# Kernel tuning notes

Measured on AMD Instinct MI355X. Metric: run time of the kernel, lower is better.

The kernel has to match this reference:

```python
import jax, jax.numpy as jnp
import numpy as np
from jax import lax


def _conv(x, w, b):
    # x: [B,C,H,W] NCHW, w: [O,I,3,3] OIHW, SAME padding, stride 1
    y = lax.conv_general_dilated(x, w, (1, 1), 'SAME',
                                 dimension_numbers=('NCHW', 'OIHW', 'NCHW'))
    return y + b[None, :, None, None]


def _maxpool2(x):
    return lax.reduce_window(x, -jnp.inf, lax.max,
                             (1, 1, 2, 2), (1, 1, 2, 2), 'VALID')


def _squash(x):
    # x: [..., D]
    norm = jnp.sum(x * x, axis=-1, keepdims=True)
    scale = norm / (1.0 + norm) / jnp.sqrt(norm + 1e-9)
    return scale * x


def _routing(x, W):
    # x: [B, R, C]  (R routes, C in_channels); W: [N, R, C, O]
    # u_hat[b,n,r,o] = sum_c x[b,r,c] * W[n,r,c,o]
    u_hat = jnp.einsum('brc,nrco->bnro', x, W)
    B, N, R, O = u_hat.shape
    b_ij = jnp.zeros((B, N, R), dtype=u_hat.dtype)
    v = None
    for it in range(3):  # fixed 3 routing iterations
        c_ij = jax.nn.softmax(b_ij, axis=2)
        s_j = jnp.einsum('bnr,bnro->bno', c_ij, u_hat)
        v = _squash(s_j)
        if it < 2:
            b_ij = b_ij + jnp.einsum('bnro,bno->bnr', u_hat, v)
    return v  # [B, N, O]


def setup_inputs() -> dict:
    key = jax.random.key(0)
    ks = jax.random.split(key, 10)
    B = 512
    num_classes = 15
    x = jax.random.normal(ks[0], (B, 3, 64, 64), dtype=jnp.float32)

    def kaiming(k, shape, fan_in):
        return jax.random.normal(k, shape, dtype=jnp.float32) * np.sqrt(2.0 / fan_in)

    w1 = kaiming(ks[1], (8, 3, 3, 3), 3 * 9)
    b1 = jnp.zeros((8,), jnp.float32)
    w2 = kaiming(ks[2], (16, 8, 3, 3), 8 * 9)
    b2 = jnp.zeros((16,), jnp.float32)
    w3 = kaiming(ks[3], (32, 16, 3, 3), 16 * 9)
    b3 = jnp.zeros((32,), jnp.float32)
    # route_weights are torch.randn in the original (std 1.0)
    rw1 = jax.random.normal(ks[4], (32, 64, 32, 8), dtype=jnp.float32)   # primary
    rw2 = jax.random.normal(ks[5], (num_classes, 32, 8, 16), dtype=jnp.float32)  # secondary
    fc_w = kaiming(ks[6], (num_classes, 16 * num_classes), 16 * num_classes)
    fc_b = jnp.zeros((num_classes,), jnp.float32)
    return {'x': x, 'w1': w1, 'b1': b1, 'w2': w2, 'b2': b2,
            'w3': w3, 'b3': b3, 'rw1': rw1, 'rw2': rw2,
            'fc_w': fc_w, 'fc_b': fc_b}


def reference(x, w1, b1, w2, b2, w3, b3, rw1, rw2, fc_w, fc_b):
    h = _maxpool2(jax.nn.relu(_conv(x, w1, b1)))   # [B,8,32,32]
    h = _maxpool2(jax.nn.relu(_conv(h, w2, b2)))   # [B,16,16,16]
    h = _maxpool2(jax.nn.relu(_conv(h, w3, b3)))   # [B,32,8,8]
    B = h.shape[0]
    # routes = 64 spatial positions, channels = 32 capsule input features
    feats = h.reshape(B, 32, 64).transpose(0, 2, 1)  # [B, 64, 32]
    v1 = _routing(feats, rw1)   # [B, 32, 8]
    v2 = _routing(v1, rw2)      # [B, 15, 16]
    flat = v2.reshape(B, -1)    # [B, 240]
    return flat @ fc_w.T + fc_b  # [B, 15]
```

## Files before the change

kernel.cpp:

```cpp
#include <hip/hip_runtime.h>
#include <hip/hip_bf16.h>


template<int CIN, int COUT, int HIN, int NO>
__global__ __launch_bounds__(256)
void conv_relu_pool(const float* __restrict__ in, const float* __restrict__ w,
                    const float* __restrict__ bias, float* __restrict__ out)
{
    constexpr int HOUT = HIN / 2;
    constexpr int PR = HIN + 2;
    constexpr int PC = (HIN + 2 + 3) & ~3;
    constexpr int NS = HIN / 8;
    constexpr int NOP = COUT / NO;
    constexpr int NTASK = NOP * HOUT * NS;
    constexpr int XWORDS = CIN * PR * PC;
    constexpr int WWORDS = CIN * 9 * COUT;

    __shared__ float xin[CIN][PR][PC];
    __shared__ float wt[WWORDS];
    __shared__ float bl[COUT];

    const int tid = threadIdx.x;
    const int b   = blockIdx.x;

    for (int i = tid; i < XWORDS; i += 256) ((float*)xin)[i] = 0.f;
    for (int i = tid; i < WWORDS; i += 256) {
        int o = i % COUT, k = (i / COUT) % 9, c = i / (COUT * 9);
        wt[i] = w[(o * CIN + c) * 9 + k];
    }
    if (tid < COUT) bl[tid] = bias[tid];
    __syncthreads();

    const float4* gin = (const float4*)(in + (size_t)b * CIN * HIN * HIN);
    constexpr int CHUNKS = CIN * HIN * (HIN / 4);
    for (int i = tid; i < CHUNKS; i += 256) {
        float4 v = gin[i];
        int ch = i % (HIN / 4);
        int y  = (i / (HIN / 4)) % HIN;
        int c  = i / ((HIN / 4) * HIN);
        float* dst = &xin[c][y + 1][ch * 4 + 1];
        dst[0] = v.x; dst[1] = v.y; dst[2] = v.z; dst[3] = v.w;
    }
    __syncthreads();

    for (int task = tid; task < NTASK; task += 256) {
        const int s  = task % NS;
        const int py = (task / NS) % HOUT;
        const int o0 = (task / (NS * HOUT)) * NO;
        const int X0 = s * 8;

        float acc[NO][2][8];
#pragma unroll
        for (int n = 0; n < NO; ++n)
#pragma unroll
            for (int q = 0; q < 2; ++q)
#pragma unroll
                for (int j = 0; j < 8; ++j) acc[n][q][j] = 0.f;

        for (int c = 0; c < CIN; ++c) {
            float rows[4][12];
#pragma unroll
            for (int rr = 0; rr < 4; ++rr) {
                const float4* src = (const float4*)&xin[c][2 * py + rr][X0];
#pragma unroll
                for (int j = 0; j < 3; ++j) {
                    float4 v = src[j];
                    rows[rr][j * 4 + 0] = v.x; rows[rr][j * 4 + 1] = v.y;
                    rows[rr][j * 4 + 2] = v.z; rows[rr][j * 4 + 3] = v.w;
                }
            }
            const float* wc = wt + c * 9 * COUT;
#pragma unroll
            for (int ky = 0; ky < 3; ++ky) {
#pragma unroll
                for (int n = 0; n < NO; ++n) {
                    const float w0 = wc[(ky * 3 + 0) * COUT + o0 + n];
                    const float w1 = wc[(ky * 3 + 1) * COUT + o0 + n];
                    const float w2 = wc[(ky * 3 + 2) * COUT + o0 + n];
#pragma unroll
                    for (int j = 0; j < 8; ++j) {
                        acc[n][0][j] = fmaf(rows[ky][j],     w0, acc[n][0][j]);
                        acc[n][0][j] = fmaf(rows[ky][j + 1], w1, acc[n][0][j]);
                        acc[n][0][j] = fmaf(rows[ky][j + 2], w2, acc[n][0][j]);
                        acc[n][1][j] = fmaf(rows[ky + 1][j],     w0, acc[n][1][j]);
                        acc[n][1][j] = fmaf(rows[ky + 1][j + 1], w1, acc[n][1][j]);
                        acc[n][1][j] = fmaf(rows[ky + 1][j + 2], w2, acc[n][1][j]);
                    }
                }
            }
        }
#pragma unroll
        for (int n = 0; n < NO; ++n) {
            const float bv = bl[o0 + n];
            float4 ov;
            float* p = (float*)&ov;
#pragma unroll
            for (int j = 0; j < 4; ++j) {
                float m = fmaxf(fmaxf(acc[n][0][2 * j], acc[n][0][2 * j + 1]),
                                fmaxf(acc[n][1][2 * j], acc[n][1][2 * j + 1]));
                p[j] = fmaxf(m + bv, 0.f);
            }
            float* po = out + (((size_t)b * COUT + o0 + n) * HOUT + py) * HOUT + s * 4;
            *(float4*)po = ov;
        }
    }
}

__global__ __launch_bounds__(256)
void transpose_w1(const float* __restrict__ W, float* __restrict__ Wt)
{
    int idx = blockIdx.x * 256 + threadIdx.x;
    if (idx >= 32 * 32 * 64 * 2) return;
    int half = idx & 1;
    int r    = (idx >> 1) & 63;
    int c    = (idx >> 7) & 31;
    int n    = idx >> 12;
    ((float4*)Wt)[idx] =
        ((const float4*)W)[(((n * 64 + r) * 32 + c) << 1) + half];
}

__global__ __launch_bounds__(256)
void routing1_einsum(const float* __restrict__ h3, const float* __restrict__ Wt,
                     float* __restrict__ uhat)
{
    constexpr int C = 32, R = 64, O = 8, G = 8;
    const int lane = threadIdx.x & 63;
    const int n    = blockIdx.y * 4 + (threadIdx.x >> 6);
    const int b0   = blockIdx.x * G;

    float u[G][O];
#pragma unroll
    for (int g = 0; g < G; ++g)
#pragma unroll
        for (int o = 0; o < O; ++o) u[g][o] = 0.f;

    const float4* wp = (const float4*)Wt + (size_t)n * C * R * 2;
    const float* xb = h3 + (size_t)b0 * (C * R) + lane;

#pragma unroll 4
    for (int c = 0; c < C; ++c) {
        float xv[G];
#pragma unroll
        for (int g = 0; g < G; ++g) xv[g] = xb[(size_t)g * (C * R) + c * R];
        float4 w0 = wp[(c * R + lane) * 2];
        float4 w1 = wp[(c * R + lane) * 2 + 1];
#pragma unroll
        for (int g = 0; g < G; ++g) {
            u[g][0] = fmaf(xv[g], w0.x, u[g][0]);
            u[g][1] = fmaf(xv[g], w0.y, u[g][1]);
            u[g][2] = fmaf(xv[g], w0.z, u[g][2]);
            u[g][3] = fmaf(xv[g], w0.w, u[g][3]);
            u[g][4] = fmaf(xv[g], w1.x, u[g][4]);
            u[g][5] = fmaf(xv[g], w1.y, u[g][5]);
            u[g][6] = fmaf(xv[g], w1.z, u[g][6]);
            u[g][7] = fmaf(xv[g], w1.w, u[g][7]);
        }
    }
#pragma unroll
    for (int g = 0; g < G; ++g) {
        float4* dst = (float4*)(uhat + (((size_t)(b0 + g) * 32 + n) * R + lane) * O);
        dst[0] = make_float4(u[g][0], u[g][1], u[g][2], u[g][3]);
        dst[1] = make_float4(u[g][4], u[g][5], u[g][6], u[g][7]);
    }
}

__global__ __launch_bounds__(256)
void routing1_iter(const float* __restrict__ uhat, float* __restrict__ v1)
{
    constexpr int O = 8;
    const int t  = threadIdx.x;
    const int b  = blockIdx.x;
    const int n  = t >> 3;
    const int rp = t & 7;

    float u[8][O];
    {
        const float4* up = (const float4*)(uhat + (((size_t)b * 32 + n) * 64 + rp * 8) * O);
#pragma unroll
        for (int i = 0; i < 16; ++i) {
            float4 w = up[i];
            u[i >> 1][(i & 1) * 4 + 0] = w.x;
            u[i >> 1][(i & 1) * 4 + 1] = w.y;
            u[i >> 1][(i & 1) * 4 + 2] = w.z;
            u[i >> 1][(i & 1) * 4 + 3] = w.w;
        }
    }

    float bij[8];
#pragma unroll
    for (int k = 0; k < 8; ++k) bij[k] = 0.f;
    float s[O];

#pragma unroll
    for (int it = 0; it < 3; ++it) {
        float e[8];
        float inv;
        if (it == 0) {
#pragma unroll
            for (int k = 0; k < 8; ++k) e[k] = 1.f;
            inv = 1.0f / 64.0f;
        } else {
            float mx = bij[0];
#pragma unroll
            for (int k = 1; k < 8; ++k) mx = fmaxf(mx, bij[k]);
#pragma unroll
            for (int m = 1; m < 8; m <<= 1) mx = fmaxf(mx, __shfl_xor(mx, m, 64));
            float sum = 0.f;
#pragma unroll
            for (int k = 0; k < 8; ++k) { e[k] = __expf(bij[k] - mx); sum += e[k]; }
#pragma unroll
            for (int m = 1; m < 8; m <<= 1) sum += __shfl_xor(sum, m, 64);
            inv = 1.f / sum;
        }
        float ta[O];
#pragma unroll
        for (int o = 0; o < O; ++o) ta[o] = 0.f;
#pragma unroll
        for (int k = 0; k < 8; ++k)
#pragma unroll
            for (int o = 0; o < O; ++o) ta[o] = fmaf(e[k], u[k][o], ta[o]);
#pragma unroll
        for (int m = 1; m < 8; m <<= 1)
#pragma unroll
            for (int o = 0; o < O; ++o) ta[o] += __shfl_xor(ta[o], m, 64);
        float nr = 0.f;
#pragma unroll
        for (int o = 0; o < O; ++o) { s[o] = ta[o] * inv; nr = fmaf(s[o], s[o], nr); }
        float scale = nr / (1.f + nr) / sqrtf(nr + 1e-9f);
#pragma unroll
        for (int o = 0; o < O; ++o) s[o] *= scale;
        if (it < 2) {
#pragma unroll
            for (int k = 0; k < 8; ++k) {
                float d = 0.f;
#pragma unroll
                for (int o = 0; o < O; ++o) d = fmaf(u[k][o], s[o], d);
                bij[k] += d;
            }
        }
    }
    float outv = s[0];
#pragma unroll
    for (int o = 1; o < O; ++o) outv = (rp == o) ? s[o] : outv;
    v1[(size_t)b * 256 + n * 8 + rp] = outv;
}

__global__ __launch_bounds__(256)
void routing2_fc(const float* __restrict__ v1, const float* __restrict__ W,
                 const float* __restrict__ fcw, const float* __restrict__ fcb,
                 float* __restrict__ out)
{
    constexpr int R = 32, C = 8, O = 16;
    __shared__ float vv[240];

    const int t  = threadIdx.x;
    const int b  = blockIdx.x;
    const int wv = t >> 6;
    const int lane = t & 63;
    const int nh = lane >> 5;
    const int r  = lane & 31;

    const float4* xr = (const float4*)(v1 + (size_t)b * 256 + r * 8);
    float4 x0 = xr[0], x1 = xr[1];
    float xv[8] = {x0.x, x0.y, x0.z, x0.w, x1.x, x1.y, x1.z, x1.w};

    float u[2][O];
    int nn[2];
#pragma unroll
    for (int p = 0; p < 2; ++p) {
        int n = wv * 4 + p * 2 + nh;
        nn[p] = n;
        int ncl = n < 15 ? n : 14;
        const float4* wp = (const float4*)(W + ((size_t)(ncl * R + r) * C) * O);
#pragma unroll
        for (int o = 0; o < O; ++o) u[p][o] = 0.f;
#pragma unroll
        for (int c = 0; c < C; ++c) {
#pragma unroll
            for (int j = 0; j < 4; ++j) {
                float4 w4 = wp[c * 4 + j];
                u[p][j * 4 + 0] = fmaf(xv[c], w4.x, u[p][j * 4 + 0]);
                u[p][j * 4 + 1] = fmaf(xv[c], w4.y, u[p][j * 4 + 1]);
                u[p][j * 4 + 2] = fmaf(xv[c], w4.z, u[p][j * 4 + 2]);
                u[p][j * 4 + 3] = fmaf(xv[c], w4.w, u[p][j * 4 + 3]);
            }
        }
    }

    float bij[2] = {0.f, 0.f};
    float s[2][O];
#pragma unroll
    for (int it = 0; it < 3; ++it) {
#pragma unroll
        for (int p = 0; p < 2; ++p) {
            float cc;
            if (it == 0) {
                cc = 1.0f / 32.0f;
            } else {
                float mx = bij[p];
#pragma unroll
                for (int w = 1; w < 32; w <<= 1) mx = fmaxf(mx, __shfl_xor(mx, w, 32));
                float e = __expf(bij[p] - mx);
                float sum = e;
#pragma unroll
                for (int w = 1; w < 32; w <<= 1) sum += __shfl_xor(sum, w, 32);
                cc = e / sum;
            }
#pragma unroll
            for (int o = 0; o < O; ++o) s[p][o] = cc * u[p][o];
        }
#pragma unroll
        for (int w = 1; w < 32; w <<= 1)
#pragma unroll
            for (int p = 0; p < 2; ++p)
#pragma unroll
                for (int o = 0; o < O; ++o) s[p][o] += __shfl_xor(s[p][o], w, 32);
#pragma unroll
        for (int p = 0; p < 2; ++p) {
            float nr = 0.f;
#pragma unroll
            for (int o = 0; o < O; ++o) nr = fmaf(s[p][o], s[p][o], nr);
            float scale = nr / (1.f + nr) / sqrtf(nr + 1e-9f);
#pragma unroll
            for (int o = 0; o < O; ++o) s[p][o] *= scale;
            if (it < 2) {
                float d = 0.f;
#pragma unroll
                for (int o = 0; o < O; ++o) d = fmaf(u[p][o], s[p][o], d);
                bij[p] += d;
            }
        }
    }
#pragma unroll
    for (int p = 0; p < 2; ++p) {
        float outv = 0.f;
#pragma unroll
        for (int o = 0; o < O; ++o) outv = (r == o) ? s[p][o] : outv;
        if (r < O && nn[p] < 15) vv[nn[p] * O + r] = outv;
    }
    __syncthreads();
    if (t < 240) {
        int j = t >> 4, k0 = t & 15;
        float acc = 0.f;
        for (int k = k0; k < 240; k += 16) acc = fmaf(vv[k], fcw[j * 240 + k], acc);
#pragma unroll
        for (int w = 1; w < 16; w <<= 1) acc += __shfl_xor(acc, w, 16);
        if (k0 == 0) out[(size_t)b * 15 + j] = acc + fcb[j];
    }
}

extern "C" void kernel_launch(void* const* d_in, const int* in_sizes, int n_in,
                              void* d_out, int out_size, void* d_ws, size_t ws_size,
                              hipStream_t stream) {
    const float* x    = (const float*)d_in[0];
    const float* w1   = (const float*)d_in[1];
    const float* b1   = (const float*)d_in[2];
    const float* w2   = (const float*)d_in[3];
    const float* b2   = (const float*)d_in[4];
    const float* w3   = (const float*)d_in[5];
    const float* b3   = (const float*)d_in[6];
    const float* rw1  = (const float*)d_in[7];
    const float* rw2  = (const float*)d_in[8];
    const float* fcw  = (const float*)d_in[9];
    const float* fcb  = (const float*)d_in[10];
    float* out = (float*)d_out;

    const int B = 512;
    float* ws = (float*)d_ws;
    float* uhat = ws;
    float* h1   = ws;
    float* h2   = h1 + (size_t)B * 8 * 32 * 32;
    float* h3   = uhat + (size_t)8388608;
    float* v1   = h3 + (size_t)B * 32 * 8 * 8;
    float* Wt   = v1 + (size_t)B * 256;

    conv_relu_pool<3, 8, 64, 4><<<B, 256, 0, stream>>>(x, w1, b1, h1);
    conv_relu_pool<8, 16, 32, 4><<<B, 256, 0, stream>>>(h1, w2, b2, h2);
    conv_relu_pool<16, 32, 16, 2><<<B, 256, 0, stream>>>(h2, w3, b3, h3);
    transpose_w1<<<(32 * 32 * 64 * 2 + 255) / 256, 256, 0, stream>>>(rw1, Wt);
    {
        dim3 grid(B / 8, 8);
        routing1_einsum<<<grid, 256, 0, stream>>>(h3, Wt, uhat);
    }
    routing1_iter<<<B, 256, 0, stream>>>(uhat, v1);
    routing2_fc<<<B, 256, 0, stream>>>(v1, rw2, fcw, fcb, out);
}
```

Before: 213.4 us.

## Split conv layers into row bands so each thread handles one task

The conv+relu+pool kernels now run on a 2D grid that splits each image into horizontal bands. Each block loads only its band of input rows plus a halo into shared memory, and each thread computes exactly one output task instead of looping over several. Conv2 also drops from four to two output channels per thread. This raises block count and cuts shared memory per block, which should help occupancy and parallelism. The cost is redundant halo loads, repeated weight staging per block, and less register reuse across output channels in conv2.

Result: slower. 228.2 us (+7.0%).

```diff
diff --git a/kernel.cpp b/kernel.cpp
--- a/kernel.cpp
+++ b/kernel.cpp
@@ -2,26 +2,27 @@
 #include <hip/hip_bf16.h>
 
 
-template<int CIN, int COUT, int HIN, int NO>
+template<int CIN, int COUT, int HIN, int NO, int BANDH>
 __global__ __launch_bounds__(256)
 void conv_relu_pool(const float* __restrict__ in, const float* __restrict__ w,
                     const float* __restrict__ bias, float* __restrict__ out)
 {
     constexpr int HOUT = HIN / 2;
-    constexpr int PR = HIN + 2;
+    constexpr int ROWS = 2 * BANDH + 2;
     constexpr int PC = (HIN + 2 + 3) & ~3;
     constexpr int NS = HIN / 8;
-    constexpr int NOP = COUT / NO;
-    constexpr int NTASK = NOP * HOUT * NS;
-    constexpr int XWORDS = CIN * PR * PC;
+    constexpr int XWORDS = CIN * ROWS * PC;
     constexpr int WWORDS = CIN * 9 * COUT;
-
-    __shared__ float xin[CIN][PR][PC];
+    static_assert((COUT / NO) * BANDH * NS == 256, "one task per thread");
+
+    __shared__ float xin[CIN][ROWS][PC];
     __shared__ float wt[WWORDS];
     __shared__ float bl[COUT];
 
-    const int tid = threadIdx.x;
-    const int b   = blockIdx.x;
+    const int tid  = threadIdx.x;
+    const int b    = blockIdx.x;
+    const int band = blockIdx.y;
+    const int y0   = 2 * (band * BANDH) - 1;
 
     for (int i = tid; i < XWORDS; i += 256) ((float*)xin)[i] = 0.f;
     for (int i = tid; i < WWORDS; i += 256) {
@@ -32,77 +33,78 @@
     __syncthreads();
 
     const float4* gin = (const float4*)(in + (size_t)b * CIN * HIN * HIN);
-    constexpr int CHUNKS = CIN * HIN * (HIN / 4);
+    constexpr int CHUNKS = CIN * ROWS * (HIN / 4);
     for (int i = tid; i < CHUNKS; i += 256) {
-        float4 v = gin[i];
         int ch = i % (HIN / 4);
-        int y  = (i / (HIN / 4)) % HIN;
-        int c  = i / ((HIN / 4) * HIN);
-        float* dst = &xin[c][y + 1][ch * 4 + 1];
-        dst[0] = v.x; dst[1] = v.y; dst[2] = v.z; dst[3] = v.w;
+        int ly = (i / (HIN / 4)) % ROWS;
+        int c  = i / ((HIN / 4) * ROWS);
+        int y  = y0 + ly;
+        if (y >= 0 && y < HIN) {
+            float4 v = gin[(c * HIN + y) * (HIN / 4) + ch];
+            float* dst = &xin[c][ly][1 + ch * 4];
+            dst[0] = v.x; dst[1] = v.y; dst[2] = v.z; dst[3] = v.w;
+        }
     }
     __syncthreads();
 
-    for (int task = tid; task < NTASK; task += 256) {
-        const int s  = task % NS;
-        const int py = (task / NS) % HOUT;
-        const int o0 = (task / (NS * HOUT)) * NO;
-        const int X0 = s * 8;
-
-        float acc[NO][2][8];
-#pragma unroll
-        for (int n = 0; n < NO; ++n)
-#pragma unroll
-            for (int q = 0; q < 2; ++q)
-#pragma unroll
-                for (int j = 0; j < 8; ++j) acc[n][q][j] = 0.f;
-
-        for (int c = 0; c < CIN; ++c) {
-            float rows[4][12];
-#pragma unroll
-            for (int rr = 0; rr < 4; ++rr) {
-                const float4* src = (const float4*)&xin[c][2 * py + rr][X0];
-#pragma unroll
-                for (int j = 0; j < 3; ++j) {
-                    float4 v = src[j];
-                    rows[rr][j * 4 + 0] = v.x; rows[rr][j * 4 + 1] = v.y;
-                    rows[rr][j * 4 + 2] = v.z; rows[rr][j * 4 + 3] = v.w;
+    const int s  = tid % NS;
+    const int py = (tid / NS) % BANDH;
+    const int o0 = (tid / (NS * BANDH)) * NO;
+    const int X0 = s * 8;
+
+    float acc[NO][2][8];
+#pragma unroll
+    for (int n = 0; n < NO; ++n)
+#pragma unroll
+        for (int q = 0; q < 2; ++q)
+#pragma unroll
+            for (int j = 0; j < 8; ++j) acc[n][q][j] = 0.f;
+
+    for (int c = 0; c < CIN; ++c) {
+        float rows[4][12];
+#pragma unroll
+        for (int rr = 0; rr < 4; ++rr) {
+            const float4* src = (const float4*)&xin[c][2 * py + rr][X0];
+#pragma unroll
+            for (int j = 0; j < 3; ++j) {
+                float4 v = src[j];
+                rows[rr][j * 4 + 0] = v.x; rows[rr][j * 4 + 1] = v.y;
+                rows[rr][j * 4 + 2] = v.z; rows[rr][j * 4 + 3] = v.w;
+            }
+        }
+        const float* wc = wt + c * 9 * COUT;
+#pragma unroll
+        for (int ky = 0; ky < 3; ++ky) {
+#pragma unroll
+            for (int n = 0; n < NO; ++n) {
+                const float w0 = wc[(ky * 3 + 0) * COUT + o0 + n];
+                const float w1 = wc[(ky * 3 + 1) * COUT + o0 + n];
+                const float w2 = wc[(ky * 3 + 2) * COUT + o0 + n];
+#pragma unroll
+                for (int j = 0; j < 8; ++j) {
+                    acc[n][0][j] = fmaf(rows[ky][j],     w0, acc[n][0][j]);
+                    acc[n][0][j] = fmaf(rows[ky][j + 1], w1, acc[n][0][j]);
+                    acc[n][0][j] = fmaf(rows[ky][j + 2], w2, acc[n][0][j]);
+                    acc[n][1][j] = fmaf(rows[ky + 1][j],     w0, acc[n][1][j]);
+                    acc[n][1][j] = fmaf(rows[ky + 1][j + 1], w1, acc[n][1][j]);
+                    acc[n][1][j] = fmaf(rows[ky + 1][j + 2], w2, acc[n][1][j]);
                 }
             }
-            const float* wc = wt + c * 9 * COUT;
-#pragma unroll
-            for (int ky = 0; ky < 3; ++ky) {
-#pragma unroll
-                for (int n = 0; n < NO; ++n) {
-                    const float w0 = wc[(ky * 3 + 0) * COUT + o0 + n];
-                    const float w1 = wc[(ky * 3 + 1) * COUT + o0 + n];
-                    const float w2 = wc[(ky * 3 + 2) * COUT + o0 + n];
-#pragma unroll
-                    for (int j = 0; j < 8; ++j) {
-                        acc[n][0][j] = fmaf(rows[ky][j],     w0, acc[n][0][j]);
-                        acc[n][0][j] = fmaf(rows[ky][j + 1], w1, acc[n][0][j]);
-                        acc[n][0][j] = fmaf(rows[ky][j + 2], w2, acc[n][0][j]);
-                        acc[n][1][j] = fmaf(rows[ky + 1][j],     w0, acc[n][1][j]);
-                        acc[n][1][j] = fmaf(rows[ky + 1][j + 1], w1, acc[n][1][j]);
-                        acc[n][1][j] = fmaf(rows[ky + 1][j + 2], w2, acc[n][1][j]);
-                    }
-                }
-            }
-        }
-#pragma unroll
-        for (int n = 0; n < NO; ++n) {
-            const float bv = bl[o0 + n];
-            float4 ov;
-            float* p = (float*)&ov;
-#pragma unroll
-            for (int j = 0; j < 4; ++j) {
-                float m = fmaxf(fmaxf(acc[n][0][2 * j], acc[n][0][2 * j + 1]),
-                                fmaxf(acc[n][1][2 * j], acc[n][1][2 * j + 1]));
-                p[j] = fmaxf(m + bv, 0.f);
-            }
-            float* po = out + (((size_t)b * COUT + o0 + n) * HOUT + py) * HOUT + s * 4;
-            *(float4*)po = ov;
-        }
+        }
+    }
+#pragma unroll
+    for (int n = 0; n < NO; ++n) {
+        const float bv = bl[o0 + n];
+        float4 ov;
+        float* p = (float*)&ov;
+#pragma unroll
+        for (int j = 0; j < 4; ++j) {
+            float m = fmaxf(fmaxf(acc[n][0][2 * j], acc[n][0][2 * j + 1]),
+                            fmaxf(acc[n][1][2 * j], acc[n][1][2 * j + 1]));
+            p[j] = fmaxf(m + bv, 0.f);
+        }
+        float* po = out + (((size_t)b * COUT + o0 + n) * HOUT + band * BANDH + py) * HOUT + s * 4;
+        *(float4*)po = ov;
     }
 }
 
@@ -374,9 +376,9 @@
     float* v1   = h3 + (size_t)B * 32 * 8 * 8;
     float* Wt   = v1 + (size_t)B * 256;
 
-    conv_relu_pool<3, 8, 64, 4><<<B, 256, 0, stream>>>(x, w1, b1, h1);
-    conv_relu_pool<8, 16, 32, 4><<<B, 256, 0, stream>>>(h1, w2, b2, h2);
-    conv_relu_pool<16, 32, 16, 2><<<B, 256, 0, stream>>>(h2, w3, b3, h3);
+    conv_relu_pool<3, 8, 64, 4, 16><<<dim3(B, 2), 256, 0, stream>>>(x, w1, b1, h1);
+    conv_relu_pool<8, 16, 32, 2, 8><<<dim3(B, 2), 256, 0, stream>>>(h1, w2, b2, h2);
+    conv_relu_pool<16, 32, 16, 2, 8><<<dim3(B, 1), 256, 0, stream>>>(h2, w3, b3, h3);
     transpose_w1<<<(32 * 32 * 64 * 2 + 255) / 256, 256, 0, stream>>>(rw1, Wt);
     {
         dim3 grid(B / 8, 8);
```

## Fuse three conv-relu-pool stages into one per-image kernel in LDS

Applied to the files above, without the earlier changes.

Replaces the three separate conv+ReLU+maxpool launches with a single kernel that keeps each image's intermediate activations in shared memory. The first conv is processed in two row bands so the input tile fits in LDS, and LDS regions are reused across stages. This removes the global-memory round trips for h1 and h2 and two kernel launches. In exchange it uses about 72KB of LDS per block, which may limit occupancy, and adds extra barriers between stages.

Result: faster. 199.1 us (-6.7%).

```diff
diff --git a/kernel.cpp b/kernel.cpp
--- a/kernel.cpp
+++ b/kernel.cpp
@@ -2,66 +2,75 @@
 #include <hip/hip_bf16.h>
 
 
-template<int CIN, int COUT, int HIN, int NO>
 __global__ __launch_bounds__(256)
-void conv_relu_pool(const float* __restrict__ in, const float* __restrict__ w,
-                    const float* __restrict__ bias, float* __restrict__ out)
+void conv_stack(const float* __restrict__ x,
+                const float* __restrict__ w1g, const float* __restrict__ b1g,
+                const float* __restrict__ w2g, const float* __restrict__ b2g,
+                const float* __restrict__ w3g, const float* __restrict__ b3g,
+                float* __restrict__ h3)
 {
-    constexpr int HOUT = HIN / 2;
-    constexpr int PR = HIN + 2;
-    constexpr int PC = (HIN + 2 + 3) & ~3;
-    constexpr int NS = HIN / 8;
-    constexpr int NOP = COUT / NO;
-    constexpr int NTASK = NOP * HOUT * NS;
-    constexpr int XWORDS = CIN * PR * PC;
-    constexpr int WWORDS = CIN * 9 * COUT;
-
-    __shared__ float xin[CIN][PR][PC];
-    __shared__ float wt[WWORDS];
-    __shared__ float bl[COUT];
+    __shared__ float lds[18152];
+    float* A  = lds;
+    float* o1 = lds + 6936;
+    float* w3 = lds + 6936;
+    float* o3 = lds + 11544;
+    float* w1 = lds + 16728;
+    float* w2 = lds + 16944;
+    float* bb = lds + 18096;
 
     const int tid = threadIdx.x;
     const int b   = blockIdx.x;
 
-    for (int i = tid; i < XWORDS; i += 256) ((float*)xin)[i] = 0.f;
-    for (int i = tid; i < WWORDS; i += 256) {
-        int o = i % COUT, k = (i / COUT) % 9, c = i / (COUT * 9);
-        wt[i] = w[(o * CIN + c) * 9 + k];
-    }
-    if (tid < COUT) bl[tid] = bias[tid];
-    __syncthreads();
-
-    const float4* gin = (const float4*)(in + (size_t)b * CIN * HIN * HIN);
-    constexpr int CHUNKS = CIN * HIN * (HIN / 4);
-    for (int i = tid; i < CHUNKS; i += 256) {
-        float4 v = gin[i];
-        int ch = i % (HIN / 4);
-        int y  = (i / (HIN / 4)) % HIN;
-        int c  = i / ((HIN / 4) * HIN);
-        float* dst = &xin[c][y + 1][ch * 4 + 1];
-        dst[0] = v.x; dst[1] = v.y; dst[2] = v.z; dst[3] = v.w;
-    }
-    __syncthreads();
-
-    for (int task = tid; task < NTASK; task += 256) {
-        const int s  = task % NS;
-        const int py = (task / NS) % HOUT;
-        const int o0 = (task / (NS * HOUT)) * NO;
-        const int X0 = s * 8;
-
-        float acc[NO][2][8];
-#pragma unroll
-        for (int n = 0; n < NO; ++n)
+    {
+        float4 z = make_float4(0.f, 0.f, 0.f, 0.f);
+        for (int i = tid; i < 4182; i += 256) ((float4*)lds)[i] = z;
+        for (int i = tid; i < 216; i += 256) {
+            int o = i % 8, k = (i / 8) % 9, c = i / 72;
+            w1[i] = w1g[(o * 3 + c) * 9 + k];
+        }
+        for (int i = tid; i < 1152; i += 256) {
+            int o = i % 16, k = (i / 16) % 9, c = i / 144;
+            w2[i] = w2g[(o * 8 + c) * 9 + k];
+        }
+        if (tid < 8)  bb[tid]      = b1g[tid];
+        if (tid < 16) bb[8 + tid]  = b2g[tid];
+        if (tid < 32) bb[24 + tid] = b3g[tid];
+    }
+    const float4* gin = (const float4*)(x + (size_t)b * 3 * 64 * 64);
+
+    auto stage_band = [&](int y0) {
+        for (int i = tid; i < 3 * 34 * 16; i += 256) {
+            int ch = i % 16;
+            int ly = (i / 16) % 34;
+            int c  = i / (16 * 34);
+            int y  = y0 + ly;
+            float4 v = make_float4(0.f, 0.f, 0.f, 0.f);
+            if (y >= 0 && y < 64) v = gin[(c * 64 + y) * 16 + ch];
+            float* d = &A[(c * 34 + ly) * 68 + 1 + ch * 4];
+            d[0] = v.x; d[1] = v.y; d[2] = v.z; d[3] = v.w;
+        }
+    };
+    stage_band(-1);
+    __syncthreads();
+
+    auto conv1_band = [&](int band) {
+        const int s  = tid & 7;
+        const int py = (tid >> 3) & 15;
+        const int og = tid >> 7;
+        const int X0 = 8 * s;
+        float acc[4][2][8];
+#pragma unroll
+        for (int n = 0; n < 4; ++n)
 #pragma unroll
             for (int q = 0; q < 2; ++q)
 #pragma unroll
                 for (int j = 0; j < 8; ++j) acc[n][q][j] = 0.f;
-
-        for (int c = 0; c < CIN; ++c) {
+#pragma unroll
+        for (int c = 0; c < 3; ++c) {
             float rows[4][12];
 #pragma unroll
             for (int rr = 0; rr < 4; ++rr) {
-                const float4* src = (const float4*)&xin[c][2 * py + rr][X0];
+                const float4* src = (const float4*)&A[(c * 34 + 2 * py + rr) * 68 + X0];
 #pragma unroll
                 for (int j = 0; j < 3; ++j) {
                     float4 v = src[j];
@@ -69,29 +78,158 @@
                     rows[rr][j * 4 + 2] = v.z; rows[rr][j * 4 + 3] = v.w;
                 }
             }
-            const float* wc = wt + c * 9 * COUT;
-#pragma unroll
-            for (int ky = 0; ky < 3; ++ky) {
-#pragma unroll
-                for (int n = 0; n < NO; ++n) {
-                    const float w0 = wc[(ky * 3 + 0) * COUT + o0 + n];
-                    const float w1 = wc[(ky * 3 + 1) * COUT + o0 + n];
-                    const float w2 = wc[(ky * 3 + 2) * COUT + o0 + n];
+            const float* wc = w1 + c * 72;
+#pragma unroll
+            for (int ky = 0; ky < 3; ++ky)
+#pragma unroll
+                for (int n = 0; n < 4; ++n) {
+                    const float q0 = wc[(ky * 3 + 0) * 8 + og * 4 + n];
+                    const float q1 = wc[(ky * 3 + 1) * 8 + og * 4 + n];
+                    const float q2 = wc[(ky * 3 + 2) * 8 + og * 4 + n];
 #pragma unroll
                     for (int j = 0; j < 8; ++j) {
-                        acc[n][0][j] = fmaf(rows[ky][j],     w0, acc[n][0][j]);
-                        acc[n][0][j] = fmaf(rows[ky][j + 1], w1, acc[n][0][j]);
-                        acc[n][0][j] = fmaf(rows[ky][j + 2], w2, acc[n][0][j]);
-                        acc[n][1][j] = fmaf(rows[ky + 1][j],     w0, acc[n][1][j]);
-                        acc[n][1][j] = fmaf(rows[ky + 1][j + 1], w1, acc[n][1][j]);
-                        acc[n][1][j] = fmaf(rows[ky + 1][j + 2], w2, acc[n][1][j]);
+                        acc[n][0][j] = fmaf(rows[ky][j],     q0, acc[n][0][j]);
+                        acc[n][0][j] = fmaf(rows[ky][j + 1], q1, acc[n][0][j]);
+                        acc[n][0][j] = fmaf(rows[ky][j + 2], q2, acc[n][0][j]);
+                        acc[n][1][j] = fmaf(rows[ky + 1][j],     q0, acc[n][1][j]);
+                        acc[n][1][j] = fmaf(rows[ky + 1][j + 1], q1, acc[n][1][j]);
+                        acc[n][1][j] = fmaf(rows[ky + 1][j + 2], q2, acc[n][1][j]);
                     }
                 }
-            }
-        }
-#pragma unroll
-        for (int n = 0; n < NO; ++n) {
-            const float bv = bl[o0 + n];
+        }
+#pragma unroll
+        for (int n = 0; n < 4; ++n) {
+            const float bv = bb[og * 4 + n];
+            const int row = 1 + band * 16 + py;
+#pragma unroll
+            for (int j = 0; j < 4; ++j) {
+                float m = fmaxf(fmaxf(acc[n][0][2 * j], acc[n][0][2 * j + 1]),
+                                fmaxf(acc[n][1][2 * j], acc[n][1][2 * j + 1]));
+                o1[((og * 4 + n) * 34 + row) * 36 + 1 + 4 * s + j] = fmaxf(m + bv, 0.f);
+            }
+        }
+    };
+    conv1_band(0);
+    __syncthreads();
+    stage_band(31);
+    __syncthreads();
+    conv1_band(1);
+    __syncthreads();
+
+    {
+        float4 z = make_float4(0.f, 0.f, 0.f, 0.f);
+        for (int i = tid; i < 1734; i += 256) ((float4*)A)[i] = z;
+    }
+    __syncthreads();
+
+    {
+        const int s  = tid & 3;
+        const int py = (tid >> 2) & 15;
+        const int og = tid >> 6;
+        const int X0 = 8 * s;
+        float acc[4][2][8];
+#pragma unroll
+        for (int n = 0; n < 4; ++n)
+#pragma unroll
+            for (int q = 0; q < 2; ++q)
+#pragma unroll
+                for (int j = 0; j < 8; ++j) acc[n][q][j] = 0.f;
+        for (int c = 0; c < 8; ++c) {
+            float rows[4][12];
+#pragma unroll
+            for (int rr = 0; rr < 4; ++rr) {
+                const float4* src = (const float4*)&o1[(c * 34 + 2 * py + rr) * 36 + X0];
+#pragma unroll
+                for (int j = 0; j < 3; ++j) {
+                    float4 v = src[j];
+                    rows[rr][j * 4 + 0] = v.x; rows[rr][j * 4 + 1] = v.y;
+                    rows[rr][j * 4 + 2] = v.z; rows[rr][j * 4 + 3] = v.w;
+                }
+            }
+            const float* wc = w2 + c * 144;
+#pragma unroll
+            for (int ky = 0; ky < 3; ++ky)
+#pragma unroll
+                for (int n = 0; n < 4; ++n) {
+                    const float q0 = wc[(ky * 3 + 0) * 16 + og * 4 + n];
+                    const float q1 = wc[(ky * 3 + 1) * 16 + og * 4 + n];
+                    const float q2 = wc[(ky * 3 + 2) * 16 + og * 4 + n];
+#pragma unroll
+                    for (int j = 0; j < 8; ++j) {
+                        acc[n][0][j] = fmaf(rows[ky][j],     q0, acc[n][0][j]);
+                        acc[n][0][j] = fmaf(rows[ky][j + 1], q1, acc[n][0][j]);
+                        acc[n][0][j] = fmaf(rows[ky][j + 2], q2, acc[n][0][j]);
+                        acc[n][1][j] = fmaf(rows[ky + 1][j],     q0, acc[n][1][j]);
+                        acc[n][1][j] = fmaf(rows[ky + 1][j + 1], q1, acc[n][1][j]);
+                        acc[n][1][j] = fmaf(rows[ky + 1][j + 2], q2, acc[n][1][j]);
+                    }
+                }
+        }
+#pragma unroll
+        for (int n = 0; n < 4; ++n) {
+            const float bv = bb[8 + og * 4 + n];
+#pragma unroll
+            for (int j = 0; j < 4; ++j) {
+                float m = fmaxf(fmaxf(acc[n][0][2 * j], acc[n][0][2 * j + 1]),
+                                fmaxf(acc[n][1][2 * j], acc[n][1][2 * j + 1]));
+                A[((og * 4 + n) * 18 + 1 + py) * 20 + 1 + 4 * s + j] = fmaxf(m + bv, 0.f);
+            }
+        }
+    }
+    __syncthreads();
+
+    for (int i = tid; i < 4608; i += 256) {
+        int o = i % 32, k = (i / 32) % 9, c = i / 288;
+        w3[i] = w3g[(o * 16 + c) * 9 + k];
+    }
+    __syncthreads();
+
+    {
+        const int s  = tid & 1;
+        const int py = (tid >> 1) & 7;
+        const int og = tid >> 4;
+        const int X0 = 8 * s;
+        float acc[2][2][8];
+#pragma unroll
+        for (int n = 0; n < 2; ++n)
+#pragma unroll
+            for (int q = 0; q < 2; ++q)
+#pragma unroll
+                for (int j = 0; j < 8; ++j) acc[n][q][j] = 0.f;
+        for (int c = 0; c < 16; ++c) {
+            float rows[4][12];
+#pragma unroll
+            for (int rr = 0; rr < 4; ++rr) {
+                const float4* src = (const float4*)&A[(c * 18 + 2 * py + rr) * 20 + X0];
+#pragma unroll
+                for (int j = 0; j < 3; ++j) {
+                    float4 v = src[j];
+                    rows[rr][j * 4 + 0] = v.x; rows[rr][j * 4 + 1] = v.y;
+                    rows[rr][j * 4 + 2] = v.z; rows[rr][j * 4 + 3] = v.w;
+                }
+            }
+            const float* wc = w3 + c * 288;
+#pragma unroll
+            for (int ky = 0; ky < 3; ++ky)
+#pragma unroll
+                for (int n = 0; n < 2; ++n) {
+                    const float q0 = wc[(ky * 3 + 0) * 32 + og * 2 + n];
+                    const float q1 = wc[(ky * 3 + 1) * 32 + og * 2 + n];
+                    const float q2 = wc[(ky * 3 + 2) * 32 + og * 2 + n];
+#pragma unroll
+                    for (int j = 0; j < 8; ++j) {
+                        acc[n][0][j] = fmaf(rows[ky][j],     q0, acc[n][0][j]);
+                        acc[n][0][j] = fmaf(rows[ky][j + 1], q1, acc[n][0][j]);
+                        acc[n][0][j] = fmaf(rows[ky][j + 2], q2, acc[n][0][j]);
+                        acc[n][1][j] = fmaf(rows[ky + 1][j],     q0, acc[n][1][j]);
+                        acc[n][1][j] = fmaf(rows[ky + 1][j + 1], q1, acc[n][1][j]);
+                        acc[n][1][j] = fmaf(rows[ky + 1][j + 2], q2, acc[n][1][j]);
+                    }
+                }
+        }
+#pragma unroll
+        for (int n = 0; n < 2; ++n) {
+            const float bv = bb[24 + og * 2 + n];
             float4 ov;
             float* p = (float*)&ov;
 #pragma unroll
@@ -100,9 +238,15 @@
                                 fmaxf(acc[n][1][2 * j], acc[n][1][2 * j + 1]));
                 p[j] = fmaxf(m + bv, 0.f);
             }
-            float* po = out + (((size_t)b * COUT + o0 + n) * HOUT + py) * HOUT + s * 4;
-            *(float4*)po = ov;
-        }
+            *(float4*)&o3[(og * 2 + n) * 64 + py * 8 + 4 * s] = ov;
+        }
+    }
+    __syncthreads();
+
+    {
+        float4* dst = (float4*)(h3 + (size_t)b * 2048);
+        const float4* src = (const float4*)o3;
+        for (int i = tid; i < 512; i += 256) dst[i] = src[i];
     }
 }
 
@@ -368,15 +512,11 @@
     const int B = 512;
     float* ws = (float*)d_ws;
     float* uhat = ws;
-    float* h1   = ws;
-    float* h2   = h1 + (size_t)B * 8 * 32 * 32;
     float* h3   = uhat + (size_t)8388608;
     float* v1   = h3 + (size_t)B * 32 * 8 * 8;
     float* Wt   = v1 + (size_t)B * 256;
 
-    conv_relu_pool<3, 8, 64, 4><<<B, 256, 0, stream>>>(x, w1, b1, h1);
-    conv_relu_pool<8, 16, 32, 4><<<B, 256, 0, stream>>>(h1, w2, b2, h2);
-    conv_relu_pool<16, 32, 16, 2><<<B, 256, 0, stream>>>(h2, w3, b3, h3);
+    conv_stack<<<B, 256, 0, stream>>>(x, w1, b1, w2, b2, w3, b3, h3);
     transpose_w1<<<(32 * 32 * 64 * 2 + 255) / 256, 256, 0, stream>>>(rw1, Wt);
     {
         dim3 grid(B / 8, 8);
```
